# Optimization experiments

Hardware: AMD Instinct MI355X
Metric: run time of the kernel (lower is better)

## Reference

```python
import jax, jax.numpy as jnp
import numpy as np
from jax import lax

B, T, F = 8, 512, 128          # batch, mel time, mel freq
DM, DS, DC, EXP, NL = 384, 16, 4, 2, 12
DI = EXP * DM                   # 768 inner width
DTR = (DM + 15) // 16           # 24, mamba_ssm dt_rank='auto'
PT = PF = 16
L = (T // PT) * (F // PF)       # 256 patches
NC = 4


def setup_inputs() -> dict:
    key = jax.random.key(0)
    ks = iter(jax.random.split(key, 24))
    def n(shape, s=0.02):
        return jax.random.normal(next(ks), shape, jnp.float32) * s
    return {
        "x": jax.random.normal(next(ks), (B, T, F), jnp.float32),
        "patch_w": n((DM, PT, PF)),
        "patch_b": jnp.zeros((DM,), jnp.float32),
        "pos_embed": n((1, L, DM)),
        "ln_g": jnp.ones((NL, DM), jnp.float32),
        "ln_b": jnp.zeros((NL, DM), jnp.float32),
        "in_proj_w": n((NL, 2 * DI, DM)),
        "conv_w": n((NL, DI, DC), 0.1),
        "conv_b": jnp.zeros((NL, DI), jnp.float32),
        "x_proj_w": n((NL, DTR + 2 * DS, DI)),
        "dt_proj_w": n((NL, DI, DTR), 0.1),
        "dt_proj_b": n((NL, DI), 0.1),
        "A_log": jnp.tile(jnp.log(jnp.arange(1, DS + 1, dtype=jnp.float32))[None, None, :], (NL, DI, 1)),
        "Dskip": jnp.ones((NL, DI), jnp.float32),
        "out_proj_w": n((NL, DM, DI)),
        "fn_g": jnp.ones((DM,), jnp.float32),
        "fn_b": jnp.zeros((DM,), jnp.float32),
        "head_w": n((NC, DM)),
        "head_b": jnp.zeros((NC,), jnp.float32),
    }


def _layernorm(x, g, b):
    m = x.mean(-1, keepdims=True)
    v = jnp.var(x, axis=-1, keepdims=True)
    return (x - m) * lax.rsqrt(v + 1e-5) * g + b


def _silu(v):
    return v * jax.nn.sigmoid(v)


def _mamba_block(x, p):
    # x: [B, L, DM]; residual Mamba block (pre-LN, dropout=identity in eval)
    ln_g, ln_b, Wi, cw, cb, Wx, Wdt, bdt, A_log, Dsk, Wo = p
    res = x
    h = _layernorm(x, ln_g, ln_b)
    xz = jnp.einsum('bld,ed->ble', h, Wi)          # [B,L,2*DI]
    u, z = jnp.split(xz, 2, axis=-1)
    # causal depthwise conv1d, kernel DC (small, unrolled)
    up = jnp.pad(u, ((0, 0), (DC - 1, 0), (0, 0)))
    u = sum(up[:, k:k + L, :] * cw[:, k] for k in range(DC)) + cb
    u = _silu(u)
    proj = jnp.einsum('bld,ed->ble', u, Wx)        # [B,L,DTR+2*DS]
    dt, Bm, Cm = jnp.split(proj, [DTR, DTR + DS], axis=-1)
    delta = jax.nn.softplus(jnp.einsum('blr,dr->bld', dt, Wdt) + bdt)  # [B,L,DI]
    A = -jnp.exp(A_log)                            # [DI, DS]
    dA = jnp.exp(delta[..., None] * A)             # [B,L,DI,DS]
    dBu = (delta * u)[..., None] * Bm[:, :, None, :]

    def step(hst, inp):
        dA_t, dBu_t, C_t = inp
        hst = dA_t * hst + dBu_t                   # [B,DI,DS]
        return hst, jnp.einsum('bdn,bn->bd', hst, C_t)

    h0 = jnp.zeros((x.shape[0], DI, DS), x.dtype)
    _, ys = lax.scan(step, h0, (dA.swapaxes(0, 1), dBu.swapaxes(0, 1), Cm.swapaxes(0, 1)))
    y = ys.swapaxes(0, 1) + u * Dsk                # [B,L,DI]
    y = y * _silu(z)
    return res + jnp.einsum('bld,ed->ble', y, Wo)


def reference(x, patch_w, patch_b, pos_embed, ln_g, ln_b, in_proj_w, conv_w, conv_b,
              x_proj_w, dt_proj_w, dt_proj_b, A_log, Dskip, out_proj_w,
              fn_g, fn_b, head_w, head_b):
    Bn = x.shape[0]
    # patch embed = non-overlapping 16x16 conv == blocked reshape + einsum
    patches = x.reshape(Bn, T // PT, PT, F // PF, PF)
    tok = jnp.einsum('bhpwq,dpq->bhwd', patches, patch_w) + patch_b
    tok = tok.reshape(Bn, L, DM) + pos_embed

    def layer(carry, p):
        return _mamba_block(carry, p), None

    tok, _ = lax.scan(layer, tok, (ln_g, ln_b, in_proj_w, conv_w, conv_b,
                                   x_proj_w, dt_proj_w, dt_proj_b, A_log, Dskip, out_proj_w))
    tok = _layernorm(tok, fn_g, fn_b)
    pooled = tok.mean(axis=1)
    return pooled @ head_w.T + head_b
```

## Files before the change

### kernel.cpp

```cpp
#include <hip/hip_runtime.h>
#include <math.h>

namespace {

constexpr int kB   = 8;
constexpr int kL   = 256;
constexpr int kTok = 2048;
constexpr int kDM  = 384;
constexpr int kDI  = 768;
constexpr int kDS  = 16;
constexpr int kDTR = 24;
constexpr int kPROJ = 56;
constexpr int kNL  = 12;

constexpr int kWIN  = 2 * kDI * kDM;
constexpr int kWOUT = kDM * kDI;
constexpr int kWX   = kPROJ * kDI;
constexpr int kWTOT = kWIN + kWOUT + kWX;

typedef float f32x4 __attribute__((ext_vector_type(4)));
typedef short short8 __attribute__((ext_vector_type(8)));

__device__ __forceinline__ float softplus_f(float x) {
  return (x > 20.f) ? x : log1pf(__expf(x));
}
__device__ __forceinline__ float silu_f(float x) {
  return x / (1.f + __expf(-x));
}
__device__ __forceinline__ unsigned short f2bf(float f) {
  union { float f; unsigned u; } v; v.f = f;
  unsigned r = v.u + 0x7FFFu + ((v.u >> 16) & 1u);
  return (unsigned short)(r >> 16);
}
__device__ __forceinline__ float bf2f(unsigned short u) {
  return __uint_as_float((unsigned)u << 16);
}

__global__ __launch_bounds__(256) void patch_gemm_k(
    const float* __restrict__ x, const float* __restrict__ Bw,
    const float* __restrict__ bias, const float* __restrict__ pos,
    float* __restrict__ C) {
  __shared__ float As[16][68];
  __shared__ float Bs[16][68];
  int tid = threadIdx.x;
  int bm = blockIdx.y * 64;
  int bn = blockIdx.x * 64;
  int lr = tid >> 2;
  int lk = (tid & 3) << 2;
  int tm = (tid >> 4) << 2;
  int tn = (tid & 15) << 2;
  float acc[4][4] = {};
  for (int k0 = 0; k0 < 256; k0 += 16) {
    {
      int token = bm + lr;
      int b = token >> 8, l = token & 255;
      int h = l >> 3, w = l & 7;
      int p = k0 >> 4;
      const float* ap = x + ((size_t)(b * 512) + h * 16 + p) * 128 + w * 16 + lk;
      float4 av = *(const float4*)ap;
      As[lk + 0][lr] = av.x; As[lk + 1][lr] = av.y;
      As[lk + 2][lr] = av.z; As[lk + 3][lr] = av.w;
    }
    {
      const float* bp = Bw + (size_t)(bn + lr) * 256 + k0 + lk;
      float4 bv = *(const float4*)bp;
      Bs[lk + 0][lr] = bv.x; Bs[lk + 1][lr] = bv.y;
      Bs[lk + 2][lr] = bv.z; Bs[lk + 3][lr] = bv.w;
    }
    __syncthreads();
    #pragma unroll
    for (int k = 0; k < 16; ++k) {
      float4 a = *(const float4*)&As[k][tm];
      float4 b = *(const float4*)&Bs[k][tn];
      float av[4] = {a.x, a.y, a.z, a.w};
      float bv[4] = {b.x, b.y, b.z, b.w};
      #pragma unroll
      for (int i = 0; i < 4; ++i)
        #pragma unroll
        for (int j = 0; j < 4; ++j)
          acc[i][j] = fmaf(av[i], bv[j], acc[i][j]);
    }
    __syncthreads();
  }
  #pragma unroll
  for (int i = 0; i < 4; ++i) {
    int row = bm + tm + i;
    #pragma unroll
    for (int j = 0; j < 4; ++j) {
      int col = bn + tn + j;
      C[(size_t)row * kDM + col] =
          acc[i][j] + bias[col] + pos[(size_t)(row & 255) * kDM + col];
    }
  }
}

template <bool BF16OUT>
__global__ __launch_bounds__(384) void ln_k(
    const float* __restrict__ in, void* __restrict__ outv,
    const float* __restrict__ g, const float* __restrict__ bb,
    float* __restrict__ proj_zero) {
  int t = blockIdx.x, d = threadIdx.x;
  if (proj_zero && d < kPROJ) proj_zero[(size_t)t * kPROJ + d] = 0.f;
  float v = in[(size_t)t * kDM + d];
  float s = v, s2 = v * v;
  #pragma unroll
  for (int m = 32; m >= 1; m >>= 1) {
    s  += __shfl_xor(s, m);
    s2 += __shfl_xor(s2, m);
  }
  __shared__ float ps[6], ps2[6];
  if ((d & 63) == 0) { ps[d >> 6] = s; ps2[d >> 6] = s2; }
  __syncthreads();
  float S = 0.f, S2 = 0.f;
  #pragma unroll
  for (int i = 0; i < 6; ++i) { S += ps[i]; S2 += ps2[i]; }
  float mean = S * (1.f / 384.f);
  float var  = S2 * (1.f / 384.f) - mean * mean;
  float r = rsqrtf(var + 1e-5f);
  float o = (v - mean) * r * g[d] + bb[d];
  if (BF16OUT) ((unsigned short*)outv)[(size_t)t * kDM + d] = f2bf(o);
  else ((float*)outv)[(size_t)t * kDM + d] = o;
}

__global__ __launch_bounds__(256) void convert_all_k(
    const float* __restrict__ w_in, const float* __restrict__ w_out,
    const float* __restrict__ w_x, unsigned short* __restrict__ dst) {
  int layer = blockIdx.y;
  int i4 = (blockIdx.x * 256 + threadIdx.x) * 4;
  if (i4 >= kWTOT) return;
  const float* src;
  int off;
  if (i4 < kWIN) { src = w_in + (size_t)layer * kWIN; off = i4; }
  else if (i4 < kWIN + kWOUT) { src = w_out + (size_t)layer * kWOUT; off = i4 - kWIN; }
  else { src = w_x + (size_t)layer * kWX; off = i4 - kWIN - kWOUT; }
  float4 v = *(const float4*)(src + off);
  unsigned short o[4] = {f2bf(v.x), f2bf(v.y), f2bf(v.z), f2bf(v.w)};
  *(uint2*)(dst + (size_t)layer * kWTOT + i4) = *(const uint2*)o;
}

template <int BN, int EPIL>
__global__ __launch_bounds__(256) void bgemm_k(
    const unsigned short* __restrict__ A, int lda,
    const unsigned short* __restrict__ B, int ldb,
    void* __restrict__ Cv, int ldc, int N, int Kc) {
  __shared__ __align__(16) unsigned short As[4][128][8];
  __shared__ __align__(16) unsigned short Bs[4][BN][8];
  int tid = threadIdx.x;
  int bm = blockIdx.y * 128;
  int bn = blockIdx.x * BN;
  int k_begin = blockIdx.z * Kc;
  int wave = tid >> 6, lane = tid & 63;
  int lm = lane & 15, lq = lane >> 4;
  int wm, wn;
  if (BN == 128) { wm = (wave >> 1) * 64; wn = (wave & 1) * 64; }
  else           { wm = wave * 32;        wn = 0; }
  constexpr int MT = (BN == 128) ? 4 : 2;
  f32x4 acc[MT][4] = {};

  for (int kt = 0; kt < Kc; kt += 32) {
    int k0 = k_begin + kt;
    int ar0 = tid & 127, aq0 = tid >> 7;
    int aq1 = aq0 + 2;
    uint4 a0 = *(const uint4*)(A + (size_t)(bm + ar0) * lda + k0 + aq0 * 8);
    uint4 a1 = *(const uint4*)(A + (size_t)(bm + ar0) * lda + k0 + aq1 * 8);
    uint4 b0, b1;
    int br0, bq0, br1 = 0, bq1 = 0;
    if (BN == 128) {
      br0 = tid & 127; bq0 = tid >> 7; br1 = br0; bq1 = bq0 + 2;
      b0 = *(const uint4*)(B + (size_t)(bn + br0) * ldb + k0 + bq0 * 8);
      b1 = *(const uint4*)(B + (size_t)(bn + br1) * ldb + k0 + bq1 * 8);
    } else {
      br0 = tid & 63; bq0 = tid >> 6;
      if (bn + br0 < N)
        b0 = *(const uint4*)(B + (size_t)(bn + br0) * ldb + k0 + bq0 * 8);
      else
        b0 = make_uint4(0u, 0u, 0u, 0u);
    }
    __syncthreads();
    *(uint4*)&As[aq0][ar0][0] = a0;
    *(uint4*)&As[aq1][ar0][0] = a1;
    *(uint4*)&Bs[bq0][br0][0] = b0;
    if (BN == 128) *(uint4*)&Bs[bq1][br1][0] = b1;
    __syncthreads();

    short8 bfrag[4];
    #pragma unroll
    for (int ni = 0; ni < 4; ++ni)
      bfrag[ni] = *(const short8*)&Bs[lq][wn + ni * 16 + lm][0];
    #pragma unroll
    for (int mi = 0; mi < MT; ++mi) {
      short8 afrag = *(const short8*)&As[lq][wm + mi * 16 + lm][0];
      #pragma unroll
      for (int ni = 0; ni < 4; ++ni)
        acc[mi][ni] = __builtin_amdgcn_mfma_f32_16x16x32_bf16(
            afrag, bfrag[ni], acc[mi][ni], 0, 0, 0);
    }
  }

  #pragma unroll
  for (int mi = 0; mi < MT; ++mi) {
    #pragma unroll
    for (int ni = 0; ni < 4; ++ni) {
      int grow0 = bm + wm + mi * 16 + lq * 4;
      int gcol = bn + wn + ni * 16 + lm;
      #pragma unroll
      for (int r = 0; r < 4; ++r) {
        float v = acc[mi][ni][r];
        int grow = grow0 + r;
        if (EPIL == 0) {
          ((float*)Cv)[(size_t)grow * ldc + gcol] = v;
        } else if (EPIL == 1) {
          if (gcol < N) atomicAdd(&((float*)Cv)[(size_t)grow * ldc + gcol], v);
        } else {
          ((unsigned short*)Cv)[(size_t)grow * ldc + gcol] = f2bf(v);
        }
      }
    }
  }
}

__global__ __launch_bounds__(256) void conv_tr_k(
    const unsigned short* __restrict__ xz, const float* __restrict__ cw,
    const float* __restrict__ cb, float* __restrict__ uT,
    unsigned short* __restrict__ sgT, unsigned short* __restrict__ u_bf) {
  int b = blockIdx.y;
  int l0 = blockIdx.x * 16;
  int tid = threadIdx.x;
  #pragma unroll
  for (int ch = 0; ch < 3; ++ch) {
    int d = ch * 256 + tid;
    float w0 = cw[d * 4], w1 = cw[d * 4 + 1], w2 = cw[d * 4 + 2], w3 = cw[d * 4 + 3];
    float bias = cb[d];
    float v[19];
    #pragma unroll
    for (int j = 0; j < 19; ++j) {
      int l = l0 - 3 + j;
      v[j] = (l >= 0) ? bf2f(xz[(size_t)(b * kL + l) * (2 * kDI) + d]) : 0.f;
    }
    float* up = uT + ((size_t)b * kDI + d) * kL + l0;
    unsigned short* sp = sgT + ((size_t)b * kDI + d) * kL + l0;
    #pragma unroll
    for (int i = 0; i < 16; ++i) {
      float acc = bias;
      acc = fmaf(v[i], w0, acc);
      acc = fmaf(v[i + 1], w1, acc);
      acc = fmaf(v[i + 2], w2, acc);
      acc = fmaf(v[i + 3], w3, acc);
      float o = silu_f(acc);
      up[i] = o;
      u_bf[(size_t)(b * kL + l0 + i) * kDI + d] = f2bf(o);
      float zv = bf2f(xz[(size_t)(b * kL + l0 + i) * (2 * kDI) + kDI + d]);
      sp[i] = f2bf(silu_f(zv));
    }
  }
}

__global__ __launch_bounds__(256) void scansplit_k(
    const float* __restrict__ proj, const float* __restrict__ uT,
    const unsigned short* __restrict__ sgT, const float* __restrict__ dtw,
    const float* __restrict__ dtb, const float* __restrict__ A_log,
    const float* __restrict__ Dsk, unsigned short* __restrict__ y_bf) {
  int d0 = blockIdx.x * 8;
  int b = blockIdx.y;
  int tid = threadIdx.x;
  int dsub = tid & 7;
  int nh = (tid >> 3) & 1;
  int c = tid >> 4;
  int d = d0 + dsub;
  __shared__ float sh[16][16][9];
  __shared__ float sca[16][16][9];

  float Av[8];
  {
    const float* ap = A_log + (size_t)d * kDS + nh * 8;
    #pragma unroll
    for (int q = 0; q < 2; ++q) {
      float4 v = ((const float4*)ap)[q];
      Av[q * 4 + 0] = -__expf(v.x);
      Av[q * 4 + 1] = -__expf(v.y);
      Av[q * 4 + 2] = -__expf(v.z);
      Av[q * 4 + 3] = -__expf(v.w);
    }
  }
  float bdt = dtb[d];
  float Dv = Dsk[d];

  const float* pr = proj + ((size_t)(b * kL) + c * 16) * kPROJ;

  float dtlo[8], dthi[8];
  {
    float wdt[24];
    const float* wp = dtw + (size_t)d * kDTR;
    #pragma unroll
    for (int q = 0; q < 6; ++q) {
      float4 v = ((const float4*)wp)[q];
      wdt[q * 4 + 0] = v.x; wdt[q * 4 + 1] = v.y;
      wdt[q * 4 + 2] = v.z; wdt[q * 4 + 3] = v.w;
    }
    const float* prm = pr + (size_t)(nh * 8) * kPROJ;
    float mine[8];
    #pragma unroll
    for (int i = 0; i < 8; ++i) {
      const float* p = prm + (size_t)i * kPROJ;
      float acc = bdt;
      #pragma unroll
      for (int q = 0; q < 6; ++q) {
        float4 v = ((const float4*)p)[q];
        acc = fmaf(v.x, wdt[q * 4 + 0], acc);
        acc = fmaf(v.y, wdt[q * 4 + 1], acc);
        acc = fmaf(v.z, wdt[q * 4 + 2], acc);
        acc = fmaf(v.w, wdt[q * 4 + 3], acc);
      }
      mine[i] = softplus_f(acc);
    }
    #pragma unroll
    for (int i = 0; i < 8; ++i) {
      float other = __shfl_xor(mine[i], 8);
      dtlo[i] = nh ? other : mine[i];
      dthi[i] = nh ? mine[i] : other;
    }
  }

  float u_[16];
  {
    const float* up = uT + ((size_t)b * kDI + d) * kL + c * 16;
    #pragma unroll
    for (int q = 0; q < 4; ++q) {
      float4 v = ((const float4*)up)[q];
      u_[q * 4 + 0] = v.x; u_[q * 4 + 1] = v.y;
      u_[q * 4 + 2] = v.z; u_[q * 4 + 3] = v.w;
    }
  }

  float h[8], ca[8];
  #pragma unroll
  for (int n = 0; n < 8; ++n) { h[n] = 0.f; ca[n] = 1.f; }
  #pragma unroll
  for (int i = 0; i < 16; ++i) {
    float dl = (i < 8) ? dtlo[i] : dthi[i - 8];
    float du = dl * u_[i];
    const float* p = pr + (size_t)i * kPROJ + 24 + nh * 8;
    float4 b0 = ((const float4*)p)[0];
    float4 b1 = ((const float4*)p)[1];
    float Bv[8] = {b0.x, b0.y, b0.z, b0.w, b1.x, b1.y, b1.z, b1.w};
    #pragma unroll
    for (int n = 0; n < 8; ++n) {
      float a = __expf(dl * Av[n]);
      h[n] = fmaf(a, h[n], du * Bv[n]);
      ca[n] *= a;
    }
  }
  {
    int nrow = nh * 8;
    #pragma unroll
    for (int q = 0; q < 8; ++q) {
      sh[c][nrow + q][dsub] = h[q];
      sca[c][nrow + q][dsub] = ca[q];
    }
  }
  __syncthreads();

  float h0[8];
  #pragma unroll
  for (int n = 0; n < 8; ++n) h0[n] = 0.f;
  {
    int nrow = nh * 8;
    for (int j = 0; j < c; ++j) {
      #pragma unroll
      for (int q = 0; q < 8; ++q)
        h0[q] = fmaf(sca[j][nrow + q][dsub], h0[q], sh[j][nrow + q][dsub]);
    }
  }

  float sg_[16];
  {
    const unsigned short* sp = sgT + ((size_t)b * kDI + d) * kL + c * 16;
    #pragma unroll
    for (int i = 0; i < 16; ++i) sg_[i] = bf2f(sp[i]);
  }

  unsigned short* yp = y_bf + (size_t)(b * kL + c * 16) * kDI + d;
  #pragma unroll
  for (int i = 0; i < 16; ++i) {
    float dl = (i < 8) ? dtlo[i] : dthi[i - 8];
    float du = dl * u_[i];
    const float* p = pr + (size_t)i * kPROJ + 24 + nh * 8;
    float4 b0 = ((const float4*)p)[0];
    float4 b1 = ((const float4*)p)[1];
    float4 c0 = ((const float4*)(p + 16))[0];
    float4 c1 = ((const float4*)(p + 16))[1];
    float Bv[8] = {b0.x, b0.y, b0.z, b0.w, b1.x, b1.y, b1.z, b1.w};
    float Cv[8] = {c0.x, c0.y, c0.z, c0.w, c1.x, c1.y, c1.z, c1.w};
    float yv = 0.f;
    #pragma unroll
    for (int n = 0; n < 8; ++n) {
      float a = __expf(dl * Av[n]);
      h0[n] = fmaf(a, h0[n], du * Bv[n]);
      yv = fmaf(h0[n], Cv[n], yv);
    }
    yv += __shfl_xor(yv, 8);
    if (nh == 0) yp[(size_t)i * kDI] = f2bf((yv + u_[i] * Dv) * sg_[i]);
  }
}

__global__ __launch_bounds__(384) void pool_k(
    const float* __restrict__ h, float* __restrict__ pooled) {
  int b = blockIdx.x, d = threadIdx.x;
  float acc = 0.f;
  for (int l = 0; l < kL; ++l) acc += h[(size_t)(b * kL + l) * kDM + d];
  pooled[b * kDM + d] = acc * (1.f / 256.f);
}

__global__ __launch_bounds__(64) void head_k(
    const float* __restrict__ pooled, const float* __restrict__ hw,
    const float* __restrict__ hb, float* __restrict__ out) {
  int b = blockIdx.x >> 2, c = blockIdx.x & 3;
  int lane = threadIdx.x;
  float acc = 0.f;
  for (int dd = lane; dd < kDM; dd += 64)
    acc = fmaf(pooled[b * kDM + dd], hw[c * kDM + dd], acc);
  #pragma unroll
  for (int m = 32; m >= 1; m >>= 1) acc += __shfl_xor(acc, m);
  if (lane == 0) out[b * 4 + c] = acc + hb[c];
}

}

extern "C" void kernel_launch(void* const* d_in, const int* in_sizes, int n_in,
                              void* d_out, int out_size, void* d_ws, size_t ws_size,
                              hipStream_t stream) {
  (void)in_sizes; (void)n_in; (void)out_size; (void)ws_size;
  const float* x        = (const float*)d_in[0];
  const float* patch_w  = (const float*)d_in[1];
  const float* patch_b  = (const float*)d_in[2];
  const float* pos      = (const float*)d_in[3];
  const float* ln_g     = (const float*)d_in[4];
  const float* ln_b     = (const float*)d_in[5];
  const float* in_w     = (const float*)d_in[6];
  const float* conv_w   = (const float*)d_in[7];
  const float* conv_b   = (const float*)d_in[8];
  const float* xproj_w  = (const float*)d_in[9];
  const float* dtproj_w = (const float*)d_in[10];
  const float* dtproj_b = (const float*)d_in[11];
  const float* A_log    = (const float*)d_in[12];
  const float* Dskip    = (const float*)d_in[13];
  const float* out_w    = (const float*)d_in[14];
  const float* fn_g     = (const float*)d_in[15];
  const float* fn_b     = (const float*)d_in[16];
  const float* head_w   = (const float*)d_in[17];
  const float* head_b   = (const float*)d_in[18];
  float* out = (float*)d_out;

  float* ws = (float*)d_ws;
  float* tok    = ws; ws += kTok * kDM;
  float* uT     = ws; ws += kTok * kDI;
  float* proj   = ws; ws += kTok * kPROJ;
  float* pooled = ws; ws += kB * kDM;
  unsigned short* xz_bf = (unsigned short*)ws; ws += kTok * 2 * kDI / 2;
  unsigned short* sgT   = (unsigned short*)ws; ws += kTok * kDI / 2;
  unsigned short* h_bf  = (unsigned short*)ws; ws += kTok * kDM / 2;
  unsigned short* y_bf  = (unsigned short*)ws; ws += kTok * kDI / 2;
  unsigned short* u_bf  = (unsigned short*)ws; ws += kTok * kDI / 2;
  unsigned short* w_bf  = (unsigned short*)ws; ws += (size_t)kNL * kWTOT / 2;
  float* lnout = uT;

  convert_all_k<<<dim3(kWTOT / 4 / 256, kNL), 256, 0, stream>>>(
      in_w, out_w, xproj_w, w_bf);

  patch_gemm_k<<<dim3(6, 32), 256, 0, stream>>>(x, patch_w, patch_b, pos, tok);

  for (int layer = 0; layer < kNL; ++layer) {
    const unsigned short* wl = w_bf + (size_t)layer * kWTOT;
    ln_k<true><<<kTok, kDM, 0, stream>>>(tok, h_bf, ln_g + layer * kDM,
                                         ln_b + layer * kDM, proj);
    bgemm_k<64, 3><<<dim3(24, 16, 1), 256, 0, stream>>>(
        h_bf, kDM, wl, kDM, xz_bf, 2 * kDI, 2 * kDI, kDM);
    conv_tr_k<<<dim3(16, kB), 256, 0, stream>>>(
        xz_bf, conv_w + layer * kDI * 4, conv_b + layer * kDI, uT, sgT, u_bf);
    bgemm_k<64, 1><<<dim3(1, 16, 6), 256, 0, stream>>>(
        u_bf, kDI, wl + kWIN + kWOUT, kDI, proj, kPROJ, kPROJ, kDI / 6);
    scansplit_k<<<dim3(kDI / 8, kB), 256, 0, stream>>>(
        proj, uT, sgT, dtproj_w + (size_t)layer * kDI * kDTR,
        dtproj_b + layer * kDI, A_log + (size_t)layer * kDI * kDS,
        Dskip + layer * kDI, y_bf);
    bgemm_k<128, 1><<<dim3(3, 16, 2), 256, 0, stream>>>(
        y_bf, kDI, wl + kWIN, kDI, tok, kDM, kDM, kDI / 2);
  }

  ln_k<false><<<kTok, kDM, 0, stream>>>(tok, lnout, fn_g, fn_b, nullptr);
  pool_k<<<kB, kDM, 0, stream>>>(lnout, pooled);
  head_k<<<kB * 4, 64, 0, stream>>>(pooled, head_w, head_b, out);
}
```

Baseline: 1.344 ms.

## Fuse layernorm into in_proj GEMM and depthwise conv into x_proj GEMM

The per-layer LayerNorm is folded into the in_proj GEMM: row statistics are computed in the prologue and the bf16 A tiles are normalized on the fly. The causal conv plus SiLU is computed inside the x_proj GEMM's A-tile load, which also writes a transposed bf16 u for the scan. The separate silu(z) buffer is dropped and the scan recomputes it from xz. This removes two kernel launches per layer and several intermediate tensors (fp32 uT, sgT, h_bf, u_bf). The cost is redundant conv work and strided transposed stores in the x_proj kernel, plus bf16 storage of u used by the scan.

```diff
diff --git a/kernel.cpp b/kernel.cpp
--- a/kernel.cpp
+++ b/kernel.cpp
@@ -94,13 +94,10 @@
   }
 }
 
-template <bool BF16OUT>
 __global__ __launch_bounds__(384) void ln_k(
-    const float* __restrict__ in, void* __restrict__ outv,
-    const float* __restrict__ g, const float* __restrict__ bb,
-    float* __restrict__ proj_zero) {
+    const float* __restrict__ in, float* __restrict__ outv,
+    const float* __restrict__ g, const float* __restrict__ bb) {
   int t = blockIdx.x, d = threadIdx.x;
-  if (proj_zero && d < kPROJ) proj_zero[(size_t)t * kPROJ + d] = 0.f;
   float v = in[(size_t)t * kDM + d];
   float s = v, s2 = v * v;
   #pragma unroll
@@ -117,9 +114,7 @@
   float mean = S * (1.f / 384.f);
   float var  = S2 * (1.f / 384.f) - mean * mean;
   float r = rsqrtf(var + 1e-5f);
-  float o = (v - mean) * r * g[d] + bb[d];
-  if (BF16OUT) ((unsigned short*)outv)[(size_t)t * kDM + d] = f2bf(o);
-  else ((float*)outv)[(size_t)t * kDM + d] = o;
+  outv[(size_t)t * kDM + d] = (v - mean) * r * g[d] + bb[d];
 }
 
 __global__ __launch_bounds__(256) void convert_all_k(
@@ -138,24 +133,212 @@
   *(uint2*)(dst + (size_t)layer * kWTOT + i4) = *(const uint2*)o;
 }
 
-template <int BN, int EPIL>
-__global__ __launch_bounds__(256) void bgemm_k(
+__global__ __launch_bounds__(256) void inproj_ln_k(
+    const float* __restrict__ tok, const unsigned short* __restrict__ Bw,
+    const float* __restrict__ g, const float* __restrict__ bb,
+    unsigned short* __restrict__ Cbf, float* __restrict__ proj_zero) {
+  __shared__ __align__(16) unsigned short As[4][128][8];
+  __shared__ __align__(16) unsigned short Bs[4][128][8];
+  __shared__ float smean[128], srstd[128];
+  __shared__ float sg_[kDM], sb_[kDM];
+  int tid = threadIdx.x;
+  int bm = blockIdx.y * 128;
+  int bn = blockIdx.x * 128;
+  {
+    int bid = blockIdx.y * 12 + blockIdx.x;
+    for (int i = bid * 256 + tid; i < kTok * kPROJ; i += 192 * 256)
+      proj_zero[i] = 0.f;
+  }
+  for (int i = tid; i < kDM; i += 256) { sg_[i] = g[i]; sb_[i] = bb[i]; }
+  {
+    int r = tid >> 1, half = tid & 1;
+    const float* rp = tok + (size_t)(bm + r) * kDM + half * 192;
+    float s = 0.f, s2 = 0.f;
+    #pragma unroll
+    for (int q = 0; q < 48; ++q) {
+      float4 v = ((const float4*)rp)[q];
+      s  += v.x + v.y + v.z + v.w;
+      s2 += v.x * v.x + v.y * v.y + v.z * v.z + v.w * v.w;
+    }
+    s  += __shfl_xor(s, 1);
+    s2 += __shfl_xor(s2, 1);
+    if (half == 0) {
+      float mean = s * (1.f / 384.f);
+      float var  = s2 * (1.f / 384.f) - mean * mean;
+      smean[r] = mean;
+      srstd[r] = rsqrtf(var + 1e-5f);
+    }
+  }
+  __syncthreads();
+  int wave = tid >> 6, lane = tid & 63;
+  int lm = lane & 15, lq = lane >> 4;
+  int wm = (wave >> 1) * 64, wn = (wave & 1) * 64;
+  f32x4 acc[4][4] = {};
+  for (int k0 = 0; k0 < kDM; k0 += 32) {
+    int ar0 = tid & 127, aq0 = tid >> 7;
+    unsigned short av[2][8];
+    float mean = smean[ar0], rstd = srstd[ar0];
+    #pragma unroll
+    for (int gq = 0; gq < 2; ++gq) {
+      int kq = aq0 + gq * 2;
+      const float* ap = tok + (size_t)(bm + ar0) * kDM + k0 + kq * 8;
+      float4 v0 = ((const float4*)ap)[0];
+      float4 v1 = ((const float4*)ap)[1];
+      float vv[8] = {v0.x, v0.y, v0.z, v0.w, v1.x, v1.y, v1.z, v1.w};
+      #pragma unroll
+      for (int j = 0; j < 8; ++j) {
+        int k = k0 + kq * 8 + j;
+        av[gq][j] = f2bf((vv[j] - mean) * rstd * sg_[k] + sb_[k]);
+      }
+    }
+    uint4 b0 = *(const uint4*)(Bw + (size_t)(bn + ar0) * kDM + k0 + aq0 * 8);
+    uint4 b1 = *(const uint4*)(Bw + (size_t)(bn + ar0) * kDM + k0 + (aq0 + 2) * 8);
+    __syncthreads();
+    *(uint4*)&As[aq0][ar0][0]     = *(const uint4*)av[0];
+    *(uint4*)&As[aq0 + 2][ar0][0] = *(const uint4*)av[1];
+    *(uint4*)&Bs[aq0][ar0][0]     = b0;
+    *(uint4*)&Bs[aq0 + 2][ar0][0] = b1;
+    __syncthreads();
+    short8 bfrag[4];
+    #pragma unroll
+    for (int ni = 0; ni < 4; ++ni)
+      bfrag[ni] = *(const short8*)&Bs[lq][wn + ni * 16 + lm][0];
+    #pragma unroll
+    for (int mi = 0; mi < 4; ++mi) {
+      short8 afrag = *(const short8*)&As[lq][wm + mi * 16 + lm][0];
+      #pragma unroll
+      for (int ni = 0; ni < 4; ++ni)
+        acc[mi][ni] = __builtin_amdgcn_mfma_f32_16x16x32_bf16(
+            afrag, bfrag[ni], acc[mi][ni], 0, 0, 0);
+    }
+  }
+  #pragma unroll
+  for (int mi = 0; mi < 4; ++mi) {
+    #pragma unroll
+    for (int ni = 0; ni < 4; ++ni) {
+      int grow0 = bm + wm + mi * 16 + lq * 4;
+      int gcol = bn + wn + ni * 16 + lm;
+      #pragma unroll
+      for (int r = 0; r < 4; ++r)
+        Cbf[(size_t)(grow0 + r) * (2 * kDI) + gcol] = f2bf(acc[mi][ni][r]);
+    }
+  }
+}
+
+__global__ __launch_bounds__(256) void xproj_conv_k(
+    const unsigned short* __restrict__ xz, const unsigned short* __restrict__ Bw,
+    const float* __restrict__ cw, const float* __restrict__ cb,
+    float* __restrict__ proj, unsigned short* __restrict__ uT_bf) {
+  __shared__ __align__(16) unsigned short As[4][128][8];
+  __shared__ __align__(16) unsigned short Bs[4][64][8];
+  __shared__ float scw[128][4];
+  __shared__ float scb[128];
+  int tid = threadIdx.x;
+  int bm = blockIdx.x * 128;
+  int kbase = blockIdx.y * 128;
+  int wave = tid >> 6, lane = tid & 63;
+  int lm = lane & 15, lq = lane >> 4;
+  int wm = wave * 32;
+  f32x4 acc[2][4] = {};
+
+  if (tid < 128) {
+    *(float4*)&scw[tid][0] = *(const float4*)(cw + (size_t)(kbase + tid) * 4);
+    scb[tid] = cb[kbase + tid];
+  }
+  __syncthreads();
+
+  int ar0 = tid & 127;
+  int aq0 = tid >> 7;
+  int t = bm + ar0;
+  int b = t >> 8, l = t & 255;
+
+  for (int kt = 0; kt < 4; ++kt) {
+    int k0 = kbase + kt * 32;
+    unsigned short av[2][8];
+    #pragma unroll
+    for (int gq = 0; gq < 2; ++gq) {
+      int kq = aq0 + gq * 2;
+      int dloc = kt * 32 + kq * 8;
+      int dg = kbase + dloc;
+      float vals[4][8];
+      #pragma unroll
+      for (int q = 0; q < 4; ++q) {
+        if (l - 3 + q >= 0) {
+          uint4 r = *(const uint4*)(xz + (size_t)(t - 3 + q) * (2 * kDI) + dg);
+          const unsigned short* rs = (const unsigned short*)&r;
+          #pragma unroll
+          for (int j = 0; j < 8; ++j) vals[q][j] = bf2f(rs[j]);
+        } else {
+          #pragma unroll
+          for (int j = 0; j < 8; ++j) vals[q][j] = 0.f;
+        }
+      }
+      #pragma unroll
+      for (int j = 0; j < 8; ++j) {
+        float a = scb[dloc + j];
+        a = fmaf(vals[0][j], scw[dloc + j][0], a);
+        a = fmaf(vals[1][j], scw[dloc + j][1], a);
+        a = fmaf(vals[2][j], scw[dloc + j][2], a);
+        a = fmaf(vals[3][j], scw[dloc + j][3], a);
+        unsigned short ub = f2bf(silu_f(a));
+        av[gq][j] = ub;
+        uT_bf[((size_t)b * kDI + dg + j) * kL + l] = ub;
+      }
+    }
+    int br0 = tid & 63, bq0 = tid >> 6;
+    uint4 b0;
+    if (br0 < kPROJ)
+      b0 = *(const uint4*)(Bw + (size_t)br0 * kDI + k0 + bq0 * 8);
+    else
+      b0 = make_uint4(0u, 0u, 0u, 0u);
+    __syncthreads();
+    *(uint4*)&As[aq0][ar0][0]     = *(const uint4*)av[0];
+    *(uint4*)&As[aq0 + 2][ar0][0] = *(const uint4*)av[1];
+    *(uint4*)&Bs[bq0][br0][0] = b0;
+    __syncthreads();
+    short8 bfrag[4];
+    #pragma unroll
+    for (int ni = 0; ni < 4; ++ni)
+      bfrag[ni] = *(const short8*)&Bs[lq][ni * 16 + lm][0];
+    #pragma unroll
+    for (int mi = 0; mi < 2; ++mi) {
+      short8 afrag = *(const short8*)&As[lq][wm + mi * 16 + lm][0];
+      #pragma unroll
+      for (int ni = 0; ni < 4; ++ni)
+        acc[mi][ni] = __builtin_amdgcn_mfma_f32_16x16x32_bf16(
+            afrag, bfrag[ni], acc[mi][ni], 0, 0, 0);
+    }
+  }
+
+  #pragma unroll
+  for (int mi = 0; mi < 2; ++mi) {
+    #pragma unroll
+    for (int ni = 0; ni < 4; ++ni) {
+      int grow0 = bm + wm + mi * 16 + lq * 4;
+      int gcol = ni * 16 + lm;
+      if (gcol < kPROJ) {
+        #pragma unroll
+        for (int r = 0; r < 4; ++r)
+          atomicAdd(&proj[(size_t)(grow0 + r) * kPROJ + gcol], acc[mi][ni][r]);
+      }
+    }
+  }
+}
+
+__global__ __launch_bounds__(256) void bgemm_out_k(
     const unsigned short* __restrict__ A, int lda,
     const unsigned short* __restrict__ B, int ldb,
-    void* __restrict__ Cv, int ldc, int N, int Kc) {
+    float* __restrict__ C, int ldc, int Kc) {
   __shared__ __align__(16) unsigned short As[4][128][8];
-  __shared__ __align__(16) unsigned short Bs[4][BN][8];
+  __shared__ __align__(16) unsigned short Bs[4][128][8];
   int tid = threadIdx.x;
   int bm = blockIdx.y * 128;
-  int bn = blockIdx.x * BN;
+  int bn = blockIdx.x * 128;
   int k_begin = blockIdx.z * Kc;
   int wave = tid >> 6, lane = tid & 63;
   int lm = lane & 15, lq = lane >> 4;
-  int wm, wn;
-  if (BN == 128) { wm = (wave >> 1) * 64; wn = (wave & 1) * 64; }
-  else           { wm = wave * 32;        wn = 0; }
-  constexpr int MT = (BN == 128) ? 4 : 2;
-  f32x4 acc[MT][4] = {};
+  int wm = (wave >> 1) * 64, wn = (wave & 1) * 64;
+  f32x4 acc[4][4] = {};
 
   for (int kt = 0; kt < Kc; kt += 32) {
     int k0 = k_begin + kt;
@@ -163,32 +346,20 @@
     int aq1 = aq0 + 2;
     uint4 a0 = *(const uint4*)(A + (size_t)(bm + ar0) * lda + k0 + aq0 * 8);
     uint4 a1 = *(const uint4*)(A + (size_t)(bm + ar0) * lda + k0 + aq1 * 8);
-    uint4 b0, b1;
-    int br0, bq0, br1 = 0, bq1 = 0;
-    if (BN == 128) {
-      br0 = tid & 127; bq0 = tid >> 7; br1 = br0; bq1 = bq0 + 2;
-      b0 = *(const uint4*)(B + (size_t)(bn + br0) * ldb + k0 + bq0 * 8);
-      b1 = *(const uint4*)(B + (size_t)(bn + br1) * ldb + k0 + bq1 * 8);
-    } else {
-      br0 = tid & 63; bq0 = tid >> 6;
-      if (bn + br0 < N)
-        b0 = *(const uint4*)(B + (size_t)(bn + br0) * ldb + k0 + bq0 * 8);
-      else
-        b0 = make_uint4(0u, 0u, 0u, 0u);
-    }
+    uint4 b0 = *(const uint4*)(B + (size_t)(bn + ar0) * ldb + k0 + aq0 * 8);
+    uint4 b1 = *(const uint4*)(B + (size_t)(bn + ar0) * ldb + k0 + aq1 * 8);
     __syncthreads();
     *(uint4*)&As[aq0][ar0][0] = a0;
     *(uint4*)&As[aq1][ar0][0] = a1;
-    *(uint4*)&Bs[bq0][br0][0] = b0;
-    if (BN == 128) *(uint4*)&Bs[bq1][br1][0] = b1;
-    __syncthreads();
-
+    *(uint4*)&Bs[aq0][ar0][0] = b0;
+    *(uint4*)&Bs[aq1][ar0][0] = b1;
+    __syncthreads();
     short8 bfrag[4];
     #pragma unroll
     for (int ni = 0; ni < 4; ++ni)
       bfrag[ni] = *(const short8*)&Bs[lq][wn + ni * 16 + lm][0];
     #pragma unroll
-    for (int mi = 0; mi < MT; ++mi) {
+    for (int mi = 0; mi < 4; ++mi) {
       short8 afrag = *(const short8*)&As[lq][wm + mi * 16 + lm][0];
       #pragma unroll
       for (int ni = 0; ni < 4; ++ni)
@@ -198,66 +369,21 @@
   }
 
   #pragma unroll
-  for (int mi = 0; mi < MT; ++mi) {
+  for (int mi = 0; mi < 4; ++mi) {
     #pragma unroll
     for (int ni = 0; ni < 4; ++ni) {
       int grow0 = bm + wm + mi * 16 + lq * 4;
       int gcol = bn + wn + ni * 16 + lm;
       #pragma unroll
-      for (int r = 0; r < 4; ++r) {
-        float v = acc[mi][ni][r];
-        int grow = grow0 + r;
-        if (EPIL == 0) {
-          ((float*)Cv)[(size_t)grow * ldc + gcol] = v;
-        } else if (EPIL == 1) {
-          if (gcol < N) atomicAdd(&((float*)Cv)[(size_t)grow * ldc + gcol], v);
-        } else {
-          ((unsigned short*)Cv)[(size_t)grow * ldc + gcol] = f2bf(v);
-        }
-      }
-    }
-  }
-}
-
-__global__ __launch_bounds__(256) void conv_tr_k(
-    const unsigned short* __restrict__ xz, const float* __restrict__ cw,
-    const float* __restrict__ cb, float* __restrict__ uT,
-    unsigned short* __restrict__ sgT, unsigned short* __restrict__ u_bf) {
-  int b = blockIdx.y;
-  int l0 = blockIdx.x * 16;
-  int tid = threadIdx.x;
-  #pragma unroll
-  for (int ch = 0; ch < 3; ++ch) {
-    int d = ch * 256 + tid;
-    float w0 = cw[d * 4], w1 = cw[d * 4 + 1], w2 = cw[d * 4 + 2], w3 = cw[d * 4 + 3];
-    float bias = cb[d];
-    float v[19];
-    #pragma unroll
-    for (int j = 0; j < 19; ++j) {
-      int l = l0 - 3 + j;
-      v[j] = (l >= 0) ? bf2f(xz[(size_t)(b * kL + l) * (2 * kDI) + d]) : 0.f;
-    }
-    float* up = uT + ((size_t)b * kDI + d) * kL + l0;
-    unsigned short* sp = sgT + ((size_t)b * kDI + d) * kL + l0;
-    #pragma unroll
-    for (int i = 0; i < 16; ++i) {
-      float acc = bias;
-      acc = fmaf(v[i], w0, acc);
-      acc = fmaf(v[i + 1], w1, acc);
-      acc = fmaf(v[i + 2], w2, acc);
-      acc = fmaf(v[i + 3], w3, acc);
-      float o = silu_f(acc);
-      up[i] = o;
-      u_bf[(size_t)(b * kL + l0 + i) * kDI + d] = f2bf(o);
-      float zv = bf2f(xz[(size_t)(b * kL + l0 + i) * (2 * kDI) + kDI + d]);
-      sp[i] = f2bf(silu_f(zv));
+      for (int r = 0; r < 4; ++r)
+        atomicAdd(&C[(size_t)(grow0 + r) * ldc + gcol], acc[mi][ni][r]);
     }
   }
 }
 
 __global__ __launch_bounds__(256) void scansplit_k(
-    const float* __restrict__ proj, const float* __restrict__ uT,
-    const unsigned short* __restrict__ sgT, const float* __restrict__ dtw,
+    const float* __restrict__ proj, const unsigned short* __restrict__ uT_bf,
+    const unsigned short* __restrict__ xz, const float* __restrict__ dtw,
     const float* __restrict__ dtb, const float* __restrict__ A_log,
     const float* __restrict__ Dsk, unsigned short* __restrict__ y_bf) {
   int d0 = blockIdx.x * 8;
@@ -323,13 +449,15 @@
 
   float u_[16];
   {
-    const float* up = uT + ((size_t)b * kDI + d) * kL + c * 16;
-    #pragma unroll
-    for (int q = 0; q < 4; ++q) {
-      float4 v = ((const float4*)up)[q];
-      u_[q * 4 + 0] = v.x; u_[q * 4 + 1] = v.y;
-      u_[q * 4 + 2] = v.z; u_[q * 4 + 3] = v.w;
-    }
+    const unsigned short* up = uT_bf + ((size_t)b * kDI + d) * kL + c * 16;
+    uint4 v0 = ((const uint4*)up)[0];
+    uint4 v1 = ((const uint4*)up)[1];
+    const unsigned short* us = (const unsigned short*)&v0;
+    #pragma unroll
+    for (int i = 0; i < 8; ++i) u_[i] = bf2f(us[i]);
+    us = (const unsigned short*)&v1;
+    #pragma unroll
+    for (int i = 0; i < 8; ++i) u_[8 + i] = bf2f(us[i]);
   }
 
   float h[8], ca[8];
@@ -373,10 +501,12 @@
   }
 
   float sg_[16];
-  {
-    const unsigned short* sp = sgT + ((size_t)b * kDI + d) * kL + c * 16;
-    #pragma unroll
-    for (int i = 0; i < 16; ++i) sg_[i] = bf2f(sp[i]);
+  if (nh == 0) {
+    const unsigned short* zp =
+        xz + (size_t)(b * kL + c * 16) * (2 * kDI) + kDI + d;
+    #pragma unroll
+    for (int i = 0; i < 16; ++i)
+      sg_[i] = silu_f(bf2f(zp[(size_t)i * (2 * kDI)]));
   }
 
   unsigned short* yp = y_bf + (size_t)(b * kL + c * 16) * kDI + d;
@@ -453,16 +583,13 @@
 
   float* ws = (float*)d_ws;
   float* tok    = ws; ws += kTok * kDM;
-  float* uT     = ws; ws += kTok * kDI;
   float* proj   = ws; ws += kTok * kPROJ;
   float* pooled = ws; ws += kB * kDM;
   unsigned short* xz_bf = (unsigned short*)ws; ws += kTok * 2 * kDI / 2;
-  unsigned short* sgT   = (unsigned short*)ws; ws += kTok * kDI / 2;
-  unsigned short* h_bf  = (unsigned short*)ws; ws += kTok * kDM / 2;
+  unsigned short* uT_bf = (unsigned short*)ws; ws += kTok * kDI / 2;
   unsigned short* y_bf  = (unsigned short*)ws; ws += kTok * kDI / 2;
-  unsigned short* u_bf  = (unsigned short*)ws; ws += kTok * kDI / 2;
   unsigned short* w_bf  = (unsigned short*)ws; ws += (size_t)kNL * kWTOT / 2;
-  float* lnout = uT;
+  float* lnout = (float*)xz_bf;
 
   convert_all_k<<<dim3(kWTOT / 4 / 256, kNL), 256, 0, stream>>>(
       in_w, out_w, xproj_w, w_bf);
@@ -471,23 +598,20 @@
 
   for (int layer = 0; layer < kNL; ++layer) {
     const unsigned short* wl = w_bf + (size_t)layer * kWTOT;
-    ln_k<true><<<kTok, kDM, 0, stream>>>(tok, h_bf, ln_g + layer * kDM,
-                                         ln_b + layer * kDM, proj);
-    bgemm_k<64, 3><<<dim3(24, 16, 1), 256, 0, stream>>>(
-        h_bf, kDM, wl, kDM, xz_bf, 2 * kDI, 2 * kDI, kDM);
-    conv_tr_k<<<dim3(16, kB), 256, 0, stream>>>(
-        xz_bf, conv_w + layer * kDI * 4, conv_b + layer * kDI, uT, sgT, u_bf);
-    bgemm_k<64, 1><<<dim3(1, 16, 6), 256, 0, stream>>>(
-        u_bf, kDI, wl + kWIN + kWOUT, kDI, proj, kPROJ, kPROJ, kDI / 6);
+    inproj_ln_k<<<dim3(12, 16), 256, 0, stream>>>(
+        tok, wl, ln_g + layer * kDM, ln_b + layer * kDM, xz_bf, proj);
+    xproj_conv_k<<<dim3(16, 6), 256, 0, stream>>>(
+        xz_bf, wl + kWIN + kWOUT, conv_w + layer * kDI * 4,
+        conv_b + layer * kDI, proj, uT_bf);
     scansplit_k<<<dim3(kDI / 8, kB), 256, 0, stream>>>(
-        proj, uT, sgT, dtproj_w + (size_t)layer * kDI * kDTR,
+        proj, uT_bf, xz_bf, dtproj_w + (size_t)layer * kDI * kDTR,
         dtproj_b + layer * kDI, A_log + (size_t)layer * kDI * kDS,
         Dskip + layer * kDI, y_bf);
-    bgemm_k<128, 1><<<dim3(3, 16, 2), 256, 0, stream>>>(
-        y_bf, kDI, wl + kWIN, kDI, tok, kDM, kDM, kDI / 2);
-  }
-
-  ln_k<false><<<kTok, kDM, 0, stream>>>(tok, lnout, fn_g, fn_b, nullptr);
+    bgemm_out_k<<<dim3(3, 16, 2), 256, 0, stream>>>(
+        y_bf, kDI, wl + kWIN, kDI, tok, kDM, kDI / 2);
+  }
+
+  ln_k<<<kTok, kDM, 0, stream>>>(tok, lnout, fn_g, fn_b);
   pool_k<<<kB, kDM, 0, stream>>>(lnout, pooled);
   head_k<<<kB * 4, 64, 0, stream>>>(pooled, head_w, head_b, out);
 }
```

Result: faster. 1.267 ms (-5.8%).
